# Performance work log

Measured on AMD Instinct MI355X. Metric: run time of the kernel, lower is better.

Reference implementation:

```python
import jax, jax.numpy as jnp
import numpy as np

NUM_HEADS = 12
TOP_K = 2
ROPE_THETA = 10000.0
EPS = 1e-6

def _rmsnorm(x, w):
    return x * jax.lax.rsqrt(jnp.mean(x * x, axis=-1, keepdims=True) + EPS) * w

def _rotate_half(t):
    t1, t2 = jnp.split(t, 2, axis=-1)
    return jnp.concatenate([-t2, t1], axis=-1)

def setup_inputs() -> dict:
    key = jax.random.key(0)
    ks = jax.random.split(key, 8)
    B, S, H, E, F = 2, 2048, 768, 8, 3072
    s = 0.02
    return {
        "x": jax.random.normal(ks[0], (B, S, H), dtype=jnp.float32),
        "attn_norm_w": jnp.ones((H,), dtype=jnp.float32),
        "wqkv": jax.random.normal(ks[1], (H, 3 * H), dtype=jnp.float32) * s,
        "wo": jax.random.normal(ks[2], (H, H), dtype=jnp.float32) * s,
        "ffn_norm_w": jnp.ones((H,), dtype=jnp.float32),
        "router_w": jax.random.normal(ks[3], (H, E), dtype=jnp.float32) * s,
        "w1": jax.random.normal(ks[4], (E, H, F), dtype=jnp.float32) * s,
        "w2": jax.random.normal(ks[5], (E, F, H), dtype=jnp.float32) * s,
    }

def reference(x, attn_norm_w, wqkv, wo, ffn_norm_w, router_w, w1, w2):
    B, S, H = x.shape
    NH, Dh = NUM_HEADS, H // NUM_HEADS
    E = router_w.shape[1]

    # ---- attention sub-block: x = x + attn(rmsnorm(x)) ----
    h = _rmsnorm(x, attn_norm_w)
    qkv = h @ wqkv  # (B,S,3H)
    q, k, v = [t.reshape(B, S, NH, Dh) for t in jnp.split(qkv, 3, axis=-1)]

    # RoPE (llama-style half-split rotation)
    half = Dh // 2
    inv_freq = 1.0 / (ROPE_THETA ** (jnp.arange(half, dtype=jnp.float32) / half))
    ang = jnp.arange(S, dtype=jnp.float32)[:, None] * inv_freq[None, :]  # (S, half)
    cos = jnp.concatenate([jnp.cos(ang)] * 2, axis=-1)[None, :, None, :].astype(x.dtype)
    sin = jnp.concatenate([jnp.sin(ang)] * 2, axis=-1)[None, :, None, :].astype(x.dtype)
    q = q * cos + _rotate_half(q) * sin
    k = k * cos + _rotate_half(k) * sin

    scores = jnp.einsum('bqhd,bkhd->bhqk', q, k) / jnp.sqrt(jnp.asarray(Dh, x.dtype))
    causal = jnp.tril(jnp.ones((S, S), dtype=bool))
    scores = jnp.where(causal[None, None], scores, jnp.asarray(-1e9, x.dtype))
    attn = jax.nn.softmax(scores, axis=-1)
    o = jnp.einsum('bhqk,bkhd->bqhd', attn, v).reshape(B, S, H) @ wo
    x = x + o

    # ---- MoE FFN sub-block: x = x + moe(rmsnorm(x)) ----
    hn = _rmsnorm(x, ffn_norm_w).reshape(-1, H)  # (T,H)
    logits = hn @ router_w  # (T,E)
    probs = jax.nn.softmax(logits, axis=-1)
    top_v, top_i = jax.lax.top_k(probs, TOP_K)  # (T,K)
    top_v = top_v / jnp.sum(top_v, axis=-1, keepdims=True)
    onehot = jax.nn.one_hot(top_i, E, dtype=x.dtype)  # (T,K,E)
    combine = jnp.einsum('tke,tk->te', onehot, top_v)  # (T,E)

    h1 = jnp.einsum('th,ehf->etf', hn, w1)
    h2 = jnp.einsum('etf,efh->eth', jax.nn.silu(h1), w2)
    moe_out = jnp.einsum('eth,te->th', h2, combine).reshape(B, S, H)

    # load-balancing aux loss (switch-style)
    frac = jnp.mean(jnp.sum(onehot, axis=1), axis=0) / TOP_K  # (E,)
    mean_prob = jnp.mean(probs, axis=0)  # (E,)
    aux = jnp.asarray(E, x.dtype) * jnp.sum(frac * mean_prob)

    return (x + moe_out, aux)
```

## Files before the change

kernel.cpp:

```cpp
#include <hip/hip_runtime.h>
#include <cstdint>
#include <cstddef>

typedef __bf16 bf16;
typedef bf16 bf16x8 __attribute__((ext_vector_type(8)));
typedef bf16 bf16x4 __attribute__((ext_vector_type(4)));
typedef float f32x4 __attribute__((ext_vector_type(4)));

static constexpr size_t SKS = (size_t)10240 * 768;

template <int N> struct ICst { static constexpr int v = N; };

__device__ __forceinline__ void async_cp16(const void* g, void* l) {
    __builtin_amdgcn_global_load_lds(
        (const __attribute__((address_space(1))) unsigned int*)(unsigned long long)g,
        (__attribute__((address_space(3))) unsigned int*)(unsigned int)(unsigned long long)l,
        16, 0, 0);
}

#define BARX() __builtin_amdgcn_s_barrier()
#define LGKM0() asm volatile("s_waitcnt lgkmcnt(0)" ::: "memory")
#define VMC8() asm volatile("s_waitcnt vmcnt(8)" ::: "memory")
#define VMC0() asm volatile("s_waitcnt vmcnt(0)" ::: "memory")

__global__ __launch_bounds__(256) void transpose_cast(const float* __restrict__ in,
                                                      bf16* __restrict__ out, int R, int C) {
    __shared__ float tile[32][33];
    int bz = blockIdx.z;
    in  += (size_t)bz * R * C;
    out += (size_t)bz * R * C;
    int c0 = blockIdx.x * 32, r0 = blockIdx.y * 32;
    int lr = threadIdx.x >> 3, lc = (threadIdx.x & 7) * 4;
    float4 v = *(const float4*)&in[(size_t)(r0 + lr) * C + c0 + lc];
    tile[lr][lc] = v.x; tile[lr][lc + 1] = v.y; tile[lr][lc + 2] = v.z; tile[lr][lc + 3] = v.w;
    __syncthreads();
    int sc = threadIdx.x >> 3, sr = (threadIdx.x & 7) * 4;
    bf16x4 o;
    o[0] = (bf16)tile[sr][sc]; o[1] = (bf16)tile[sr + 1][sc];
    o[2] = (bf16)tile[sr + 2][sc]; o[3] = (bf16)tile[sr + 3][sc];
    *(bf16x4*)&out[(size_t)(c0 + sc) * R + r0 + sr] = o;
}

__global__ __launch_bounds__(256) void rmsnorm_cast(const float* __restrict__ x,
                                                    const float* __restrict__ w,
                                                    bf16* __restrict__ out) {
    int row = blockIdx.x, tid = threadIdx.x;
    const float* xr = x + (size_t)row * 768;
    float v0 = xr[tid], v1 = xr[tid + 256], v2 = xr[tid + 512];
    float s = v0 * v0 + v1 * v1 + v2 * v2;
#pragma unroll
    for (int off = 32; off; off >>= 1) s += __shfl_xor(s, off, 64);
    __shared__ float red[4];
    if ((tid & 63) == 0) red[tid >> 6] = s;
    __syncthreads();
    float tot = red[0] + red[1] + red[2] + red[3];
    float rs = rsqrtf(tot * (1.f / 768.f) + 1e-6f);
    bf16* o = out + (size_t)row * 768;
    o[tid]       = (bf16)(v0 * rs * w[tid]);
    o[tid + 256] = (bf16)(v1 * rs * w[tid + 256]);
    o[tid + 512] = (bf16)(v2 * rs * w[tid + 512]);
}

__global__ __launch_bounds__(256) void rope_kernel(const bf16* __restrict__ qkv,
                                                   bf16* __restrict__ qb,
                                                   bf16* __restrict__ kb,
                                                   bf16* __restrict__ vtb) {
    __shared__ float vs[64][65];
    const int tid = threadIdx.x;
    const int s0 = blockIdx.x * 64, bh = blockIdx.y;
    const int b = bh / 12, h = bh - b * 12;
    const float qscale = 0.18033688f;
#pragma unroll
    for (int i = 0; i < 16; ++i) {
        int idx = i * 256 + tid;
        int sl = idx >> 6, d = idx & 63;
        int sg = s0 + sl;
        size_t base = ((size_t)b * 2048 + sg) * 2304;
        float qv = (float)qkv[base + h * 64 + d];
        float kv = (float)qkv[base + 768 + h * 64 + d];
        float vv = (float)qkv[base + 1536 + h * 64 + d];
        float qp = (float)qkv[base + h * 64 + (d ^ 32)];
        float kp = (float)qkv[base + 768 + h * 64 + (d ^ 32)];
        int jj = d & 31;
        float invf = __expf(-(float)jj * (9.210340371976184f / 32.f));
        float ang = (float)sg * invf;
        float cv, sv;
        __sincosf(ang, &sv, &cv);
        float rq = (d < 32) ? -qp : qp;
        float rk = (d < 32) ? -kp : kp;
        qb[((size_t)bh * 2048 + sg) * 64 + d] = (bf16)((qv * cv + rq * sv) * qscale);
        kb[((size_t)bh * 2048 + sg) * 64 + d] = (bf16)(kv * cv + rk * sv);
        vs[sl][d] = vv;
    }
    __syncthreads();
#pragma unroll
    for (int i = 0; i < 16; ++i) {
        int idx = i * 256 + tid;
        int d = idx >> 6, sl = idx & 63;
        vtb[(size_t)bh * 64 * 2048 + (size_t)d * 2048 + s0 + sl] = (bf16)vs[sl][d];
    }
}

__global__ __launch_bounds__(256) void attn_kernel(const bf16* __restrict__ qb,
                                                   const bf16* __restrict__ kb,
                                                   const bf16* __restrict__ vtb,
                                                   bf16* __restrict__ ob) {
    __shared__ __align__(16) bf16 Qs[2][64][32];
    __shared__ __align__(16) bf16 Ks[2][2][64][32];
    __shared__ __align__(16) bf16 Vts[2][2][64][32];
    __shared__ __align__(16) bf16 Ps[4][1024];

    const int tid = threadIdx.x, lane = tid & 63, w = tid >> 6;
    const int quad = lane >> 4, l16 = lane & 15;
    const int linear = (int)blockIdx.y * 32 + (int)blockIdx.x;
    const int xcd = linear & 7, j = linear >> 3;
    const int bh = xcd * 3 + (j >> 5);
    const int qt = 31 - (j & 31);
    const int q0 = qt * 64;
    const int b = bh / 12, h = bh - b * 12;

    const bf16* qhead = qb + (size_t)bh * 2048 * 64;
    const bf16* khead = kb + (size_t)bh * 2048 * 64;
    const bf16* vthead = vtb + (size_t)bh * 64 * 2048;

#pragma unroll
    for (int i = 0; i < 2; ++i) {
        int o = (i * 256 + tid) * 16;
        int kk = o >> 12, row = (o >> 6) & 63, el = (o & 63) >> 1;
        async_cp16(qhead + (size_t)(q0 + row) * 64 + kk * 32 + el,
                   (char*)Qs + (size_t)(i * 256 + w * 64) * 16);
    }
    __syncthreads();
    bf16x8 bq[2];
#pragma unroll
    for (int kk = 0; kk < 2; ++kk)
        bq[kk] = *(const bf16x8*)&Qs[kk][w * 16 + l16][quad * 8];

    f32x4 o_acc[4] = {};
    float m_st = -1e30f, l_st = 0.f;

    for (int j2 = 0; j2 <= qt; j2 += 2) {
        int nt2 = (j2 + 1 <= qt) ? 2 : 1;
        __syncthreads();
#pragma unroll
        for (int t = 0; t < 2; ++t) {
            if (t >= nt2) break;
            int kv0 = (j2 + t) * 64;
#pragma unroll
            for (int i = 0; i < 2; ++i) {
                int o = (i * 256 + tid) * 16;
                int kk = o >> 12, row = (o >> 6) & 63, el = (o & 63) >> 1;
                async_cp16(khead + (size_t)(kv0 + row) * 64 + kk * 32 + el,
                           (char*)&Ks[t] + (size_t)(i * 256 + w * 64) * 16);
                async_cp16(vthead + (size_t)row * 2048 + kv0 + kk * 32 + el,
                           (char*)&Vts[t] + (size_t)(i * 256 + w * 64) * 16);
            }
        }
        __syncthreads();

#pragma unroll
        for (int t = 0; t < 2; ++t) {
            if (t >= nt2) break;

            f32x4 sacc[4] = {};
#pragma unroll
            for (int kk = 0; kk < 2; ++kk) {
                bf16x8 ak[4];
#pragma unroll
                for (int ni = 0; ni < 4; ++ni)
                    ak[ni] = *(const bf16x8*)&Ks[t][kk][ni * 16 + l16][quad * 8];
#pragma unroll
                for (int ni = 0; ni < 4; ++ni)
                    sacc[ni] = __builtin_amdgcn_mfma_f32_16x16x32_bf16(ak[ni], bq[kk], sacc[ni], 0, 0, 0);
            }

            if (j2 + t == qt) {
                int ql = w * 16 + l16;
#pragma unroll
                for (int ni = 0; ni < 4; ++ni)
#pragma unroll
                    for (int r = 0; r < 4; ++r)
                        if (ni * 16 + quad * 4 + r > ql) sacc[ni][r] = -1e30f;
            }

            float mx = sacc[0][0];
#pragma unroll
            for (int ni = 0; ni < 4; ++ni)
#pragma unroll
                for (int r = 0; r < 4; ++r) mx = fmaxf(mx, sacc[ni][r]);
            mx = fmaxf(mx, __shfl_xor(mx, 16, 64));
            mx = fmaxf(mx, __shfl_xor(mx, 32, 64));
            float mnew = fmaxf(m_st, mx);
            float alpha = exp2f(m_st - mnew);
            m_st = mnew;
            float rsum = 0.f;
#pragma unroll
            for (int ni = 0; ni < 4; ++ni)
#pragma unroll
                for (int r = 0; r < 4; ++r) {
                    float pv = exp2f(sacc[ni][r] - mnew);
                    sacc[ni][r] = pv;
                    rsum += pv;
                }
            rsum += __shfl_xor(rsum, 16, 64);
            rsum += __shfl_xor(rsum, 32, 64);
            l_st = l_st * alpha + rsum;

            float af[4];
#pragma unroll
            for (int r = 0; r < 4; ++r) af[r] = __shfl(alpha, quad * 4 + r, 64);
#pragma unroll
            for (int ni = 0; ni < 4; ++ni)
#pragma unroll
                for (int r = 0; r < 4; ++r) o_acc[ni][r] *= af[r];

            bf16* pb = Ps[w];
#pragma unroll
            for (int ni = 0; ni < 4; ++ni)
#pragma unroll
                for (int r = 0; r < 4; ++r) {
                    int kv = ni * 16 + quad * 4 + r;
                    int ch = (kv >> 3) ^ (l16 & 7);
                    pb[l16 * 64 + ch * 8 + (kv & 7)] = (bf16)sacc[ni][r];
                }

#pragma unroll
            for (int kk = 0; kk < 2; ++kk) {
                int ch = (kk * 4 + quad) ^ (l16 & 7);
                bf16x8 ap = *(const bf16x8*)&pb[l16 * 64 + ch * 8];
                bf16x8 bv[4];
#pragma unroll
                for (int ni = 0; ni < 4; ++ni)
                    bv[ni] = *(const bf16x8*)&Vts[t][kk][ni * 16 + l16][quad * 8];
#pragma unroll
                for (int ni = 0; ni < 4; ++ni)
                    o_acc[ni] = __builtin_amdgcn_mfma_f32_16x16x32_bf16(ap, bv[ni], o_acc[ni], 0, 0, 0);
            }
        }
    }

    float lf[4];
#pragma unroll
    for (int r = 0; r < 4; ++r) lf[r] = 1.f / __shfl(l_st, quad * 4 + r, 64);
#pragma unroll
    for (int ni = 0; ni < 4; ++ni)
#pragma unroll
        for (int r = 0; r < 4; ++r) {
            int rowg = q0 + w * 16 + quad * 4 + r;
            size_t tk = (size_t)b * 2048 + rowg;
            ob[tk * 768 + h * 64 + ni * 16 + l16] = (bf16)(o_acc[ni][r] * lf[r]);
        }
}

__global__ __launch_bounds__(256) void rms_router(const float* __restrict__ x1,
                                                  const float* __restrict__ w,
                                                  const float* __restrict__ rw,
                                                  bf16* __restrict__ hn,
                                                  int* __restrict__ topi,
                                                  float* __restrict__ topw,
                                                  float* __restrict__ probsb) {
    __shared__ float hnf[768];
    __shared__ float part[256];
    __shared__ float lg[8];
    __shared__ float probs[8];
    __shared__ float red[4];
    int row = blockIdx.x, tid = threadIdx.x;
    const float* xr = x1 + (size_t)row * 768;
    float v0 = xr[tid], v1 = xr[tid + 256], v2 = xr[tid + 512];
    float s = v0 * v0 + v1 * v1 + v2 * v2;
#pragma unroll
    for (int off = 32; off; off >>= 1) s += __shfl_xor(s, off, 64);
    if ((tid & 63) == 0) red[tid >> 6] = s;
    __syncthreads();
    float tot = red[0] + red[1] + red[2] + red[3];
    float rs = rsqrtf(tot * (1.f / 768.f) + 1e-6f);
    float h0 = v0 * rs * w[tid], h1v = v1 * rs * w[tid + 256], h2v = v2 * rs * w[tid + 512];
    hnf[tid] = h0; hnf[tid + 256] = h1v; hnf[tid + 512] = h2v;
    bf16* o = hn + (size_t)row * 768;
    o[tid] = (bf16)h0; o[tid + 256] = (bf16)h1v; o[tid + 512] = (bf16)h2v;
    __syncthreads();
    int e = tid & 7, seg = tid >> 3;
    float p = 0.f;
#pragma unroll
    for (int j = 0; j < 24; ++j) { int k = seg * 24 + j; p += hnf[k] * rw[k * 8 + e]; }
    part[tid] = p;
    __syncthreads();
    if (tid < 8) { float a = 0.f; for (int sgi = 0; sgi < 32; ++sgi) a += part[sgi * 8 + tid]; lg[tid] = a; }
    __syncthreads();
    if (tid == 0) {
        float mx = lg[0];
        for (int i = 1; i < 8; ++i) mx = fmaxf(mx, lg[i]);
        float ssum = 0.f, ex[8];
        for (int i = 0; i < 8; ++i) { ex[i] = __expf(lg[i] - mx); ssum += ex[i]; }
        float inv = 1.f / ssum;
        for (int i = 0; i < 8; ++i) probs[i] = ex[i] * inv;
        int e0 = 0; float p0 = probs[0];
        for (int i = 1; i < 8; ++i) if (probs[i] > p0) { p0 = probs[i]; e0 = i; }
        int e1 = -1; float p1 = -1.f;
        for (int i = 0; i < 8; ++i) if (i != e0 && probs[i] > p1) { p1 = probs[i]; e1 = i; }
        float wsum = p0 + p1;
        topi[row * 2] = e0; topi[row * 2 + 1] = e1;
        topw[row * 2] = p0 / wsum; topw[row * 2 + 1] = p1 / wsum;
    }
    __syncthreads();
    if (tid < 8) probsb[(size_t)row * 8 + tid] = probs[tid];
}

__global__ __launch_bounds__(256) void router_stats(const float* __restrict__ probsb,
                                                    const int* __restrict__ topi,
                                                    int* ctrl, int4* tiles, float* auxOut) {
    __shared__ float pws[4][8];
    __shared__ int cws[4][8];
    int tid = threadIdx.x;
    float s[8] = {};
    int cnt[8] = {};
    for (int t = tid; t < 4096; t += 256) {
        const float4* p = (const float4*)(probsb + (size_t)t * 8);
        float4 a = p[0], b = p[1];
        s[0] += a.x; s[1] += a.y; s[2] += a.z; s[3] += a.w;
        s[4] += b.x; s[5] += b.y; s[6] += b.z; s[7] += b.w;
        int e0 = topi[2 * t], e1 = topi[2 * t + 1];
#pragma unroll
        for (int e = 0; e < 8; ++e) cnt[e] += (e == e0) + (e == e1);
    }
#pragma unroll
    for (int e = 0; e < 8; ++e)
#pragma unroll
        for (int off = 32; off; off >>= 1) {
            s[e] += __shfl_xor(s[e], off, 64);
            cnt[e] += __shfl_xor(cnt[e], off, 64);
        }
    if ((tid & 63) == 0) {
#pragma unroll
        for (int e = 0; e < 8; ++e) { pws[tid >> 6][e] = s[e]; cws[tid >> 6][e] = cnt[e]; }
    }
    __syncthreads();
    if (tid == 0) {
        int off = 0, nt = 0;
        float aux = 0.f;
        for (int e = 0; e < 8; ++e) {
            int ne = cws[0][e] + cws[1][e] + cws[2][e] + cws[3][e];
            float ps = pws[0][e] + pws[1][e] + pws[2][e] + pws[3][e];
            ctrl[e] = ne;
            ctrl[32 + e] = off;
            int ntl = (ne + 255) >> 8;
            for (int i = 0; i < ntl; ++i) { tiles[nt] = make_int4(e, off + i * 256, off + ne, 0); ++nt; }
            off += ntl << 8;
            aux += ((float)ne * (1.f / 8192.f)) * (ps * (1.f / 4096.f));
        }
        ctrl[24] = nt;
        auxOut[0] = 8.f * aux;
    }
}

__global__ __launch_bounds__(256) void place_tokens(const int* __restrict__ topi,
                                                    int* ctrl, int* __restrict__ perm,
                                                    int* __restrict__ tokslot) {
    __shared__ int lcnt[8], lbase[8];
    int tid = threadIdx.x;
    int t = blockIdx.x * 256 + tid;
    if (tid < 8) lcnt[tid] = 0;
    __syncthreads();
    int e0 = topi[2 * t], e1 = topi[2 * t + 1];
    int p0 = atomicAdd(&lcnt[e0], 1);
    int p1 = atomicAdd(&lcnt[e1], 1);
    __syncthreads();
    if (tid < 8) lbase[tid] = atomicAdd(&ctrl[16 + tid], lcnt[tid]);
    __syncthreads();
    int g0 = ctrl[32 + e0] + lbase[e0] + p0;
    int g1 = ctrl[32 + e1] + lbase[e1] + p1;
    perm[g0] = t; perm[g1] = t;
    tokslot[2 * t] = g0; tokslot[2 * t + 1] = g1;
}

__global__ __launch_bounds__(192) void moe_combine(const float* __restrict__ h2p,
                                                   const int* __restrict__ tokslot,
                                                   const float* __restrict__ topw,
                                                   float* __restrict__ out) {
    int t = blockIdx.x, tid = threadIdx.x;
    int s0 = tokslot[2 * t], s1 = tokslot[2 * t + 1];
    float w0 = topw[2 * t], w1 = topw[2 * t + 1];
    int c = tid * 4;
    float4 a0 = *(const float4*)(h2p + (size_t)s0 * 768 + c);
    float4 a1 = *(const float4*)(h2p + SKS + (size_t)s0 * 768 + c);
    float4 b0 = *(const float4*)(h2p + (size_t)s1 * 768 + c);
    float4 b1 = *(const float4*)(h2p + SKS + (size_t)s1 * 768 + c);
    float4* o = (float4*)(out + (size_t)t * 768 + c);
    float4 ov = *o;
    ov.x += w0 * (a0.x + a1.x) + w1 * (b0.x + b1.x);
    ov.y += w0 * (a0.y + a1.y) + w1 * (b0.y + b1.y);
    ov.z += w0 * (a0.z + a1.z) + w1 * (b0.z + b1.z);
    ov.w += w0 * (a0.w + a1.w) + w1 * (b0.w + b1.w);
    *o = ov;
}

template <int MODE, int KTOT, int SK>
__global__ __launch_bounds__(512, 2) void gemm8p(const bf16* __restrict__ A,
                                                 const bf16* __restrict__ Bt,
                                                 int N,
                                                 bf16* __restrict__ outB,
                                                 float* __restrict__ outF,
                                                 const int4* __restrict__ tiles,
                                                 const int* __restrict__ ctrl,
                                                 const int* __restrict__ perm) {
    constexpr int KB = KTOT / SK;
    constexpr int nT = KB >> 6;
    __shared__ __align__(16) bf16 As[2][2][128 * 64];
    __shared__ __align__(16) bf16 Bs[2][2][128 * 64];
    __shared__ int sPerm[256];

    const int tid = threadIdx.x, lane = tid & 63, wid = tid >> 6;
    const int wr = wid >> 2, wc = wid & 3;
    const int quad = lane >> 4, l16 = lane & 15;

    const int NB = N >> 8;
    const int nwg = (int)gridDim.x, q8 = nwg >> 3;
    const int L = (int)blockIdx.x;
    const int lin = (L & 7) * q8 + (L >> 3);
    int mt, nb, sk = 0;
    if (SK == 2) { int d = NB * 2; mt = lin / d; int r = lin - mt * d; nb = r >> 1; sk = r & 1; }
    else         { mt = lin / NB; nb = lin - mt * NB; }
    const int n0 = nb << 8;
    const int k0 = sk * KB;

    int m0 = 0, row0 = 0;
    if (MODE == 0) {
        m0 = mt << 8;
    } else {
        if (mt >= ctrl[24]) return;
        int4 td = tiles[mt];
        row0 = td.y;
        Bt += (size_t)td.x * (size_t)N * KTOT;
        if (MODE == 2) {
            if (tid < 256) {
                int g = row0 + tid;
                sPerm[tid] = perm[(g < td.z) ? g : row0];
            }
            __syncthreads();
        }
    }

    const int r0t = tid >> 3, s0t = tid & 7;
    const int cOff = ((s0t ^ (r0t & 7)) << 3);
    unsigned aOff[2][2], bOff[2][2];
#pragma unroll
    for (int h = 0; h < 2; ++h)
#pragma unroll
        for (int i = 0; i < 2; ++i) {
            int rrow = h * 128 + i * 64 + r0t;
            bOff[h][i] = (unsigned)((((n0 + rrow) * KTOT) + k0 + cOff) * 2);
            int ar = (MODE == 0) ? (m0 + rrow) : (MODE == 2 ? sPerm[rrow] : row0 + rrow);
            aOff[h][i] = (unsigned)(((ar * KTOT) + k0 + cOff) * 2);
        }
    const char* Ab = (const char*)A;
    const char* Bb = (const char*)Bt;

    auto stA = [&](int buf, int ktB) {
#pragma unroll
        for (int h = 0; h < 2; ++h)
#pragma unroll
            for (int i = 0; i < 2; ++i)
                async_cp16(Ab + aOff[h][i] + ktB,
                           (char*)As[buf][h] + (size_t)((i * 512 + wid * 64) * 16));
    };
    auto stB = [&](int buf, int ktB) {
#pragma unroll
        for (int h = 0; h < 2; ++h)
#pragma unroll
            for (int i = 0; i < 2; ++i)
                async_cp16(Bb + bOff[h][i] + ktB,
                           (char*)Bs[buf][h] + (size_t)((i * 512 + wid * 64) * 16));
    };

    const bf16* aP[2][2];
    const bf16* bP[2][2];
#pragma unroll
    for (int bb = 0; bb < 2; ++bb)
#pragma unroll
        for (int kk = 0; kk < 2; ++kk) {
            int swz = ((kk * 4 + quad) ^ (l16 & 7)) * 8;
            aP[bb][kk] = (const bf16*)As[bb][wr] + l16 * 64 + swz;
            bP[bb][kk] = (const bf16*)Bs[bb][wc >> 1] + ((wc & 1) * 64 + l16) * 64 + swz;
        }

    f32x4 acc[8][4] = {};
    bf16x8 aLo[4][2], aHi[4][2], bLo[2][2], bHi[2][2];

    stA(0, 0); stB(0, 0); stA(1, 128); stB(1, 128);
    VMC8();
    BARX();

    auto dotile = [&](auto BC, int t) {
        constexpr int b = decltype(BC)::v;
        const bool st = (t + 2 < nT);
        const int ktB = (t + 2) << 7;

#pragma unroll
        for (int mi = 0; mi < 4; ++mi) {
            aLo[mi][0] = *(const bf16x8*)(aP[b][0] + mi * 1024);
            aLo[mi][1] = *(const bf16x8*)(aP[b][1] + mi * 1024);
        }
#pragma unroll
        for (int ni = 0; ni < 2; ++ni) {
            bLo[ni][0] = *(const bf16x8*)(bP[b][0] + ni * 1024);
            bLo[ni][1] = *(const bf16x8*)(bP[b][1] + ni * 1024);
        }
        BARX(); LGKM0();
        __builtin_amdgcn_s_setprio(1);
#pragma unroll
        for (int mi = 0; mi < 4; ++mi)
#pragma unroll
            for (int ni = 0; ni < 2; ++ni) {
                acc[mi][ni] = __builtin_amdgcn_mfma_f32_16x16x32_bf16(aLo[mi][0], bLo[ni][0], acc[mi][ni], 0, 0, 0);
                acc[mi][ni] = __builtin_amdgcn_mfma_f32_16x16x32_bf16(aLo[mi][1], bLo[ni][1], acc[mi][ni], 0, 0, 0);
            }
        __builtin_amdgcn_s_setprio(0);
        BARX();

#pragma unroll
        for (int ni = 0; ni < 2; ++ni) {
            bHi[ni][0] = *(const bf16x8*)(bP[b][0] + (ni + 2) * 1024);
            bHi[ni][1] = *(const bf16x8*)(bP[b][1] + (ni + 2) * 1024);
        }
        BARX(); LGKM0();
        __builtin_amdgcn_s_setprio(1);
#pragma unroll
        for (int mi = 0; mi < 4; ++mi)
#pragma unroll
            for (int ni = 0; ni < 2; ++ni) {
                acc[mi][ni + 2] = __builtin_amdgcn_mfma_f32_16x16x32_bf16(aLo[mi][0], bHi[ni][0], acc[mi][ni + 2], 0, 0, 0);
                acc[mi][ni + 2] = __builtin_amdgcn_mfma_f32_16x16x32_bf16(aLo[mi][1], bHi[ni][1], acc[mi][ni + 2], 0, 0, 0);
            }
        __builtin_amdgcn_s_setprio(0);
        BARX();

#pragma unroll
        for (int mi = 0; mi < 4; ++mi) {
            aHi[mi][0] = *(const bf16x8*)(aP[b][0] + (mi + 4) * 1024);
            aHi[mi][1] = *(const bf16x8*)(aP[b][1] + (mi + 4) * 1024);
        }
        if (st) stB(b, ktB);
        BARX(); LGKM0();
        __builtin_amdgcn_s_setprio(1);
#pragma unroll
        for (int mi = 0; mi < 4; ++mi)
#pragma unroll
            for (int ni = 0; ni < 2; ++ni) {
                acc[mi + 4][ni + 2] = __builtin_amdgcn_mfma_f32_16x16x32_bf16(aHi[mi][0], bHi[ni][0], acc[mi + 4][ni + 2], 0, 0, 0);
                acc[mi + 4][ni + 2] = __builtin_amdgcn_mfma_f32_16x16x32_bf16(aHi[mi][1], bHi[ni][1], acc[mi + 4][ni + 2], 0, 0, 0);
            }
        __builtin_amdgcn_s_setprio(0);
        BARX();

        if (st) stA(b, ktB);
        BARX();
        __builtin_amdgcn_s_setprio(1);
#pragma unroll
        for (int mi = 0; mi < 4; ++mi)
#pragma unroll
            for (int ni = 0; ni < 2; ++ni) {
                acc[mi + 4][ni] = __builtin_amdgcn_mfma_f32_16x16x32_bf16(aHi[mi][0], bLo[ni][0], acc[mi + 4][ni], 0, 0, 0);
                acc[mi + 4][ni] = __builtin_amdgcn_mfma_f32_16x16x32_bf16(aHi[mi][1], bLo[ni][1], acc[mi + 4][ni], 0, 0, 0);
            }
        __builtin_amdgcn_s_setprio(0);
        if (st) { VMC8(); } else if (t + 2 == nT) { VMC0(); }
        BARX();
    };

    for (int t = 0; t < nT; t += 2) {
        dotile(ICst<0>{}, t);
        dotile(ICst<1>{}, t + 1);
    }

#pragma unroll
    for (int mi = 0; mi < 8; ++mi)
#pragma unroll
        for (int ni = 0; ni < 4; ++ni)
#pragma unroll
            for (int r = 0; r < 4; ++r) {
                int lrow = wr * 128 + mi * 16 + quad * 4 + r;
                int col  = n0 + wc * 64 + ni * 16 + l16;
                float v = acc[mi][ni][r];
                if (MODE == 0) {
                    outB[(size_t)(m0 + lrow) * N + col] = (bf16)v;
                } else if (MODE == 2) {
                    float sv = v / (1.f + __expf(-v));
                    outB[(size_t)(row0 + lrow) * N + col] = (bf16)sv;
                } else {
                    outF[(size_t)sk * SKS + (size_t)(row0 + lrow) * N + col] = v;
                }
            }
}

template <int MODE, int NBX, int MTX>
__global__ __launch_bounds__(256) void gemm_nt(const bf16* __restrict__ A,
                                               const bf16* __restrict__ Bt,
                                               int N, int K,
                                               const float* __restrict__ xres,
                                               float* __restrict__ outF,
                                               bf16* __restrict__ outB) {
    __shared__ __align__(16) bf16 As[2][128 * 32];
    __shared__ __align__(16) bf16 Bs[2][128 * 32];

    const int tid = threadIdx.x, lane = tid & 63, w = tid >> 6;
    const int wr = w >> 1, wc = w & 1, quad = lane >> 4, l16 = lane & 15;

    const int L = blockIdx.x;
    const int xcd = L & 7, j = L >> 3;
    const int mt = xcd * MTX + j / NBX;
    const int n0 = (j % NBX) * 128;
    const int m0 = mt * 128;

    auto stage = [&](int buf, int kt) {
#pragma unroll
        for (int i = 0; i < 2; ++i) {
            int c = i * 256 + tid;
            int r = c >> 2, koff = (c & 3) * 8;
            async_cp16(A + (size_t)(m0 + r) * K + kt + koff,
                       (char*)As[buf] + (size_t)(i * 256 + w * 64) * 16);
            async_cp16(Bt + (size_t)(n0 + r) * K + kt + koff,
                       (char*)Bs[buf] + (size_t)(i * 256 + w * 64) * 16);
        }
    };

    f32x4 acc[4][4] = {};
    const int nIt = K >> 5;
    stage(0, 0);

    for (int it = 0; it < nIt; ++it) {
        const int cur = it & 1;
        __syncthreads();
        if (it + 1 < nIt) stage(cur ^ 1, (it + 1) << 5);

        bf16x8 af[4], bfr[4];
#pragma unroll
        for (int mi = 0; mi < 4; ++mi)
            af[mi] = *(const bf16x8*)(As[cur] + (wr * 64 + mi * 16 + l16) * 32 + quad * 8);
#pragma unroll
        for (int ni = 0; ni < 4; ++ni)
            bfr[ni] = *(const bf16x8*)(Bs[cur] + (wc * 64 + ni * 16 + l16) * 32 + quad * 8);
#pragma unroll
        for (int mi = 0; mi < 4; ++mi)
#pragma unroll
            for (int ni = 0; ni < 4; ++ni)
                acc[mi][ni] = __builtin_amdgcn_mfma_f32_16x16x32_bf16(af[mi], bfr[ni], acc[mi][ni], 0, 0, 0);
    }

#pragma unroll
    for (int mi = 0; mi < 4; ++mi)
#pragma unroll
        for (int ni = 0; ni < 4; ++ni)
#pragma unroll
            for (int r = 0; r < 4; ++r) {
                int lrow = wr * 64 + mi * 16 + quad * 4 + r;
                int col = n0 + wc * 64 + ni * 16 + l16;
                float v = acc[mi][ni][r];
                if (MODE == 1) {
                    size_t idx = (size_t)(m0 + lrow) * N + col;
                    outF[idx] = v + xres[idx];
                } else {
                    outB[(size_t)(m0 + lrow) * N + col] = (bf16)v;
                }
            }
}

__global__ void zero_ctrl(int* ctrl) { if (threadIdx.x < 64) ctrl[threadIdx.x] = 0; }

extern "C" void kernel_launch(void* const* d_in, const int* in_sizes, int n_in,
                              void* d_out, int out_size, void* d_ws, size_t ws_size,
                              hipStream_t stream) {
    const float* x    = (const float*)d_in[0];
    const float* anw  = (const float*)d_in[1];
    const float* wqkv = (const float*)d_in[2];
    const float* wo   = (const float*)d_in[3];
    const float* fnw  = (const float*)d_in[4];
    const float* rw   = (const float*)d_in[5];
    const float* w1   = (const float*)d_in[6];
    const float* w2   = (const float*)d_in[7];
    float* out = (float*)d_out;

    char* ws = (char*)d_ws;
    size_t off = 0;
    auto alloc = [&](size_t bytes) -> char* {
        char* p = ws + off;
        off = (off + bytes + 255) & ~(size_t)255;
        return p;
    };
    bf16* wqkvT = (bf16*)alloc(2304ull * 768 * 2);
    bf16* woT   = (bf16*)alloc(768ull * 768 * 2);
    bf16* w2T   = (bf16*)alloc(8ull * 768 * 3072 * 2);
    bf16* w1T   = (bf16*)alloc(8ull * 3072 * 768 * 2);
    bf16* hbuf  = (bf16*)alloc(4096ull * 768 * 2);
    bf16* qkvb  = (bf16*)alloc(4096ull * 2304 * 2);
    bf16* qb    = (bf16*)alloc(24ull * 2048 * 64 * 2);
    bf16* kb    = (bf16*)alloc(24ull * 2048 * 64 * 2);
    bf16* vtb   = (bf16*)alloc(24ull * 64 * 2048 * 2);
    bf16* obuf  = (bf16*)alloc(4096ull * 768 * 2);
    bf16* hn    = (bf16*)alloc(4096ull * 768 * 2);
    int*  topi  = (int*)alloc(4096ull * 2 * 4);
    float* topw = (float*)alloc(4096ull * 2 * 4);
    float* probsb = (float*)alloc(4096ull * 8 * 4);
    int*  ctrl  = (int*)alloc(64 * 4);
    int4* tiles = (int4*)alloc(80 * 16);
    int*  perm  = (int*)alloc(10240 * 4);
    int*  tokslot = (int*)alloc(4096ull * 2 * 4);
    bf16* h1    = (bf16*)alloc(10240ull * 3072 * 2);
    float* h2p  = (float*)w1T;
    (void)ws_size; (void)in_sizes; (void)n_in;

    zero_ctrl<<<1, 64, 0, stream>>>(ctrl);
    transpose_cast<<<dim3(72, 24, 1), 256, 0, stream>>>(wqkv, wqkvT, 768, 2304);
    transpose_cast<<<dim3(24, 24, 1), 256, 0, stream>>>(wo, woT, 768, 768);
    transpose_cast<<<dim3(96, 24, 8), 256, 0, stream>>>(w1, w1T, 768, 3072);
    transpose_cast<<<dim3(24, 96, 8), 256, 0, stream>>>(w2, w2T, 3072, 768);
    rmsnorm_cast<<<4096, 256, 0, stream>>>(x, anw, hbuf);
    gemm8p<0, 768, 1><<<144, 512, 0, stream>>>(hbuf, wqkvT, 2304, qkvb, nullptr,
                                               nullptr, nullptr, nullptr);
    rope_kernel<<<dim3(32, 24), 256, 0, stream>>>(qkvb, qb, kb, vtb);
    attn_kernel<<<dim3(32, 24), 256, 0, stream>>>(qb, kb, vtb, obuf);
    gemm_nt<1, 6, 4><<<192, 256, 0, stream>>>(obuf, woT, 768, 768, x, out, nullptr);
    rms_router<<<4096, 256, 0, stream>>>(out, fnw, rw, hn, topi, topw, probsb);
    router_stats<<<1, 256, 0, stream>>>(probsb, topi, ctrl, tiles, out + (out_size - 1));
    place_tokens<<<16, 256, 0, stream>>>(topi, ctrl, perm, tokslot);
    gemm8p<2, 768, 1><<<480, 512, 0, stream>>>(hn, w1T, 3072, h1, nullptr,
                                               tiles, ctrl, perm);
    gemm8p<3, 3072, 2><<<240, 512, 0, stream>>>(h1, w2T, 768, nullptr, h2p,
                                                tiles, ctrl, perm);
    moe_combine<<<4096, 192, 0, stream>>>(h2p, tokslot, topw, out);
}
```

Measured before the change: 500.2 us.

## Load GEMM A operand directly into registers, stage only B through LDS

The 256x256 GEMM kernel stops staging the A tile through shared memory. Each wave now reads its A rows straight from global memory into registers, one k-step ahead, while B keeps its double-buffered async LDS copies. The per-tile schedule shrinks to two MFMA phases with fewer barriers. Workgroup swizzling is dropped for the MoE modes. This removes LDS traffic and barriers for A, but adds register pressure (16 bf16x8 A fragments live per wave) and exposes global-load latency, since A is fetched with uncoalesced 16-byte per-lane reads right before use.

```diff
diff --git a/kernel.cpp b/kernel.cpp
--- a/kernel.cpp
+++ b/kernel.cpp
@@ -19,8 +19,8 @@
 }
 
 #define BARX() __builtin_amdgcn_s_barrier()
-#define LGKM0() asm volatile("s_waitcnt lgkmcnt(0)" ::: "memory")
-#define VMC8() asm volatile("s_waitcnt vmcnt(8)" ::: "memory")
+#define SBAR0() __builtin_amdgcn_sched_barrier(0)
+#define VMC4() asm volatile("s_waitcnt vmcnt(4)" ::: "memory")
 #define VMC0() asm volatile("s_waitcnt vmcnt(0)" ::: "memory")
 
 __global__ __launch_bounds__(256) void transpose_cast(const float* __restrict__ in,
@@ -395,7 +395,7 @@
 }
 
 template <int MODE, int KTOT, int SK>
-__global__ __launch_bounds__(512, 2) void gemm8p(const bf16* __restrict__ A,
+__global__ __launch_bounds__(512, 2) void gemm2p(const bf16* __restrict__ A,
                                                  const bf16* __restrict__ Bt,
                                                  int N,
                                                  bf16* __restrict__ outB,
@@ -405,7 +405,6 @@
                                                  const int* __restrict__ perm) {
     constexpr int KB = KTOT / SK;
     constexpr int nT = KB >> 6;
-    __shared__ __align__(16) bf16 As[2][2][128 * 64];
     __shared__ __align__(16) bf16 Bs[2][2][128 * 64];
     __shared__ int sPerm[256];
 
@@ -414,9 +413,14 @@
     const int quad = lane >> 4, l16 = lane & 15;
 
     const int NB = N >> 8;
-    const int nwg = (int)gridDim.x, q8 = nwg >> 3;
     const int L = (int)blockIdx.x;
-    const int lin = (L & 7) * q8 + (L >> 3);
+    int lin;
+    if (MODE == 0) {
+        const int q8 = (int)gridDim.x >> 3;
+        lin = (L & 7) * q8 + (L >> 3);
+    } else {
+        lin = L;
+    }
     int mt, nb, sk = 0;
     if (SK == 2) { int d = NB * 2; mt = lin / d; int r = lin - mt * d; nb = r >> 1; sk = r & 1; }
     else         { mt = lin / NB; nb = lin - mt * NB; }
@@ -442,27 +446,16 @@
 
     const int r0t = tid >> 3, s0t = tid & 7;
     const int cOff = ((s0t ^ (r0t & 7)) << 3);
-    unsigned aOff[2][2], bOff[2][2];
+    unsigned bOff[2][2];
 #pragma unroll
     for (int h = 0; h < 2; ++h)
 #pragma unroll
         for (int i = 0; i < 2; ++i) {
             int rrow = h * 128 + i * 64 + r0t;
             bOff[h][i] = (unsigned)((((n0 + rrow) * KTOT) + k0 + cOff) * 2);
-            int ar = (MODE == 0) ? (m0 + rrow) : (MODE == 2 ? sPerm[rrow] : row0 + rrow);
-            aOff[h][i] = (unsigned)(((ar * KTOT) + k0 + cOff) * 2);
-        }
-    const char* Ab = (const char*)A;
+        }
     const char* Bb = (const char*)Bt;
 
-    auto stA = [&](int buf, int ktB) {
-#pragma unroll
-        for (int h = 0; h < 2; ++h)
-#pragma unroll
-            for (int i = 0; i < 2; ++i)
-                async_cp16(Ab + aOff[h][i] + ktB,
-                           (char*)As[buf][h] + (size_t)((i * 512 + wid * 64) * 16));
-    };
     auto stB = [&](int buf, int ktB) {
 #pragma unroll
         for (int h = 0; h < 2; ++h)
@@ -472,99 +465,88 @@
                            (char*)Bs[buf][h] + (size_t)((i * 512 + wid * 64) * 16));
     };
 
-    const bf16* aP[2][2];
     const bf16* bP[2][2];
 #pragma unroll
     for (int bb = 0; bb < 2; ++bb)
 #pragma unroll
         for (int kk = 0; kk < 2; ++kk) {
             int swz = ((kk * 4 + quad) ^ (l16 & 7)) * 8;
-            aP[bb][kk] = (const bf16*)As[bb][wr] + l16 * 64 + swz;
             bP[bb][kk] = (const bf16*)Bs[bb][wc >> 1] + ((wc & 1) * 64 + l16) * 64 + swz;
         }
 
+    const char* aPtr[8];
+#pragma unroll
+    for (int mi = 0; mi < 8; ++mi) {
+        int lrow = wr * 128 + mi * 16 + l16;
+        int rowIdx = (MODE == 0) ? (m0 + lrow) : (MODE == 2 ? sPerm[lrow] : row0 + lrow);
+        aPtr[mi] = (const char*)A + (size_t)((unsigned)rowIdx * (unsigned)KTOT + (unsigned)(k0 + quad * 8)) * 2;
+    }
+
     f32x4 acc[8][4] = {};
-    bf16x8 aLo[4][2], aHi[4][2], bLo[2][2], bHi[2][2];
-
-    stA(0, 0); stB(0, 0); stA(1, 128); stB(1, 128);
-    VMC8();
-    BARX();
+    bf16x8 aCur[8][2];
+
+    auto loadA = [&](int ktB) {
+#pragma unroll
+        for (int mi = 0; mi < 8; ++mi)
+#pragma unroll
+            for (int kk = 0; kk < 2; ++kk)
+                aCur[mi][kk] = *(const bf16x8*)(aPtr[mi] + ktB + kk * 64);
+    };
+
+    stB(0, 0);
+    SBAR0();
+    loadA(0);
+    SBAR0();
+    stB(1, 128);
+    SBAR0();
 
     auto dotile = [&](auto BC, int t) {
         constexpr int b = decltype(BC)::v;
-        const bool st = (t + 2 < nT);
-        const int ktB = (t + 2) << 7;
-
-#pragma unroll
-        for (int mi = 0; mi < 4; ++mi) {
-            aLo[mi][0] = *(const bf16x8*)(aP[b][0] + mi * 1024);
-            aLo[mi][1] = *(const bf16x8*)(aP[b][1] + mi * 1024);
-        }
+        const bool lastT = (t == nT - 1);
+
+        if (lastT) { VMC0(); } else { VMC4(); }
+        BARX();
+        SBAR0();
+
+        bf16x8 bLo[2][2];
 #pragma unroll
         for (int ni = 0; ni < 2; ++ni) {
             bLo[ni][0] = *(const bf16x8*)(bP[b][0] + ni * 1024);
             bLo[ni][1] = *(const bf16x8*)(bP[b][1] + ni * 1024);
         }
-        BARX(); LGKM0();
         __builtin_amdgcn_s_setprio(1);
 #pragma unroll
-        for (int mi = 0; mi < 4; ++mi)
+        for (int mi = 0; mi < 8; ++mi)
 #pragma unroll
             for (int ni = 0; ni < 2; ++ni) {
-                acc[mi][ni] = __builtin_amdgcn_mfma_f32_16x16x32_bf16(aLo[mi][0], bLo[ni][0], acc[mi][ni], 0, 0, 0);
-                acc[mi][ni] = __builtin_amdgcn_mfma_f32_16x16x32_bf16(aLo[mi][1], bLo[ni][1], acc[mi][ni], 0, 0, 0);
+                acc[mi][ni] = __builtin_amdgcn_mfma_f32_16x16x32_bf16(aCur[mi][0], bLo[ni][0], acc[mi][ni], 0, 0, 0);
+                acc[mi][ni] = __builtin_amdgcn_mfma_f32_16x16x32_bf16(aCur[mi][1], bLo[ni][1], acc[mi][ni], 0, 0, 0);
             }
         __builtin_amdgcn_s_setprio(0);
-        BARX();
-
+
+        bf16x8 bHi[2][2];
 #pragma unroll
         for (int ni = 0; ni < 2; ++ni) {
             bHi[ni][0] = *(const bf16x8*)(bP[b][0] + (ni + 2) * 1024);
             bHi[ni][1] = *(const bf16x8*)(bP[b][1] + (ni + 2) * 1024);
         }
-        BARX(); LGKM0();
         __builtin_amdgcn_s_setprio(1);
 #pragma unroll
-        for (int mi = 0; mi < 4; ++mi)
+        for (int mi = 0; mi < 8; ++mi)
 #pragma unroll
             for (int ni = 0; ni < 2; ++ni) {
-                acc[mi][ni + 2] = __builtin_amdgcn_mfma_f32_16x16x32_bf16(aLo[mi][0], bHi[ni][0], acc[mi][ni + 2], 0, 0, 0);
-                acc[mi][ni + 2] = __builtin_amdgcn_mfma_f32_16x16x32_bf16(aLo[mi][1], bHi[ni][1], acc[mi][ni + 2], 0, 0, 0);
+                acc[mi][ni + 2] = __builtin_amdgcn_mfma_f32_16x16x32_bf16(aCur[mi][0], bHi[ni][0], acc[mi][ni + 2], 0, 0, 0);
+                acc[mi][ni + 2] = __builtin_amdgcn_mfma_f32_16x16x32_bf16(aCur[mi][1], bHi[ni][1], acc[mi][ni + 2], 0, 0, 0);
             }
         __builtin_amdgcn_s_setprio(0);
+
+        SBAR0();
         BARX();
-
-#pragma unroll
-        for (int mi = 0; mi < 4; ++mi) {
-            aHi[mi][0] = *(const bf16x8*)(aP[b][0] + (mi + 4) * 1024);
-            aHi[mi][1] = *(const bf16x8*)(aP[b][1] + (mi + 4) * 1024);
-        }
-        if (st) stB(b, ktB);
-        BARX(); LGKM0();
-        __builtin_amdgcn_s_setprio(1);
-#pragma unroll
-        for (int mi = 0; mi < 4; ++mi)
-#pragma unroll
-            for (int ni = 0; ni < 2; ++ni) {
-                acc[mi + 4][ni + 2] = __builtin_amdgcn_mfma_f32_16x16x32_bf16(aHi[mi][0], bHi[ni][0], acc[mi + 4][ni + 2], 0, 0, 0);
-                acc[mi + 4][ni + 2] = __builtin_amdgcn_mfma_f32_16x16x32_bf16(aHi[mi][1], bHi[ni][1], acc[mi + 4][ni + 2], 0, 0, 0);
-            }
-        __builtin_amdgcn_s_setprio(0);
-        BARX();
-
-        if (st) stA(b, ktB);
-        BARX();
-        __builtin_amdgcn_s_setprio(1);
-#pragma unroll
-        for (int mi = 0; mi < 4; ++mi)
-#pragma unroll
-            for (int ni = 0; ni < 2; ++ni) {
-                acc[mi + 4][ni] = __builtin_amdgcn_mfma_f32_16x16x32_bf16(aHi[mi][0], bLo[ni][0], acc[mi + 4][ni], 0, 0, 0);
-                acc[mi + 4][ni] = __builtin_amdgcn_mfma_f32_16x16x32_bf16(aHi[mi][1], bLo[ni][1], acc[mi + 4][ni], 0, 0, 0);
-            }
-        __builtin_amdgcn_s_setprio(0);
-        if (st) { VMC8(); } else if (t + 2 == nT) { VMC0(); }
-        BARX();
+        if (!lastT) {
+            loadA((t + 1) << 7);
+            SBAR0();
+            if (t + 2 < nT) { stB(b, (t + 2) << 7); SBAR0(); }
+        }
     };
 
     for (int t = 0; t < nT; t += 2) {
@@ -714,7 +696,7 @@
     transpose_cast<<<dim3(96, 24, 8), 256, 0, stream>>>(w1, w1T, 768, 3072);
     transpose_cast<<<dim3(24, 96, 8), 256, 0, stream>>>(w2, w2T, 3072, 768);
     rmsnorm_cast<<<4096, 256, 0, stream>>>(x, anw, hbuf);
-    gemm8p<0, 768, 1><<<144, 512, 0, stream>>>(hbuf, wqkvT, 2304, qkvb, nullptr,
+    gemm2p<0, 768, 1><<<144, 512, 0, stream>>>(hbuf, wqkvT, 2304, qkvb, nullptr,
                                                nullptr, nullptr, nullptr);
     rope_kernel<<<dim3(32, 24), 256, 0, stream>>>(qkvb, qb, kb, vtb);
     attn_kernel<<<dim3(32, 24), 256, 0, stream>>>(qb, kb, vtb, obuf);
@@ -722,9 +704,9 @@
     rms_router<<<4096, 256, 0, stream>>>(out, fnw, rw, hn, topi, topw, probsb);
     router_stats<<<1, 256, 0, stream>>>(probsb, topi, ctrl, tiles, out + (out_size - 1));
     place_tokens<<<16, 256, 0, stream>>>(topi, ctrl, perm, tokslot);
-    gemm8p<2, 768, 1><<<480, 512, 0, stream>>>(hn, w1T, 3072, h1, nullptr,
+    gemm2p<2, 768, 1><<<480, 512, 0, stream>>>(hn, w1T, 3072, h1, nullptr,
                                                tiles, ctrl, perm);
-    gemm8p<3, 3072, 2><<<240, 512, 0, stream>>>(h1, w2T, 768, nullptr, h2p,
+    gemm2p<3, 3072, 2><<<240, 512, 0, stream>>>(h1, w2T, 768, nullptr, h2p,
                                                 tiles, ctrl, perm);
     moe_combine<<<4096, 192, 0, stream>>>(h2p, tokslot, topw, out);
 }
```

After: 699.2 us. +39.8%, slower.

## Fuse prep kernels and overlap expert weight transposes with attention

Applied to the files above, without the earlier changes.

Merges the zero-ctrl, wqkv/wo transpose-casts and the first rmsnorm into a single launch. The large w1/w2 expert-weight transpose-cast blocks are appended to the attention grid, so the bandwidth-bound conversion can fill CUs left idle by the causal, imbalanced attention blocks. This cuts several launches and hides the weight conversion behind attention. The risk is that the many transpose blocks compete with attention for bandwidth and CU slots, and the shared-memory union may lower attention occupancy.

```diff
diff --git a/kernel.cpp b/kernel.cpp
--- a/kernel.cpp
+++ b/kernel.cpp
@@ -23,42 +23,54 @@
 #define VMC8() asm volatile("s_waitcnt vmcnt(8)" ::: "memory")
 #define VMC0() asm volatile("s_waitcnt vmcnt(0)" ::: "memory")
 
-__global__ __launch_bounds__(256) void transpose_cast(const float* __restrict__ in,
-                                                      bf16* __restrict__ out, int R, int C) {
-    __shared__ float tile[32][33];
-    int bz = blockIdx.z;
-    in  += (size_t)bz * R * C;
-    out += (size_t)bz * R * C;
-    int c0 = blockIdx.x * 32, r0 = blockIdx.y * 32;
-    int lr = threadIdx.x >> 3, lc = (threadIdx.x & 7) * 4;
+__device__ __forceinline__ void tc_body(const float* __restrict__ in, bf16* __restrict__ out,
+                                        int R, int C, int r0, int c0, float* shf) {
+    float (*tile)[33] = (float(*)[33])shf;
+    int tid = threadIdx.x;
+    int lr = tid >> 3, lc = (tid & 7) * 4;
     float4 v = *(const float4*)&in[(size_t)(r0 + lr) * C + c0 + lc];
     tile[lr][lc] = v.x; tile[lr][lc + 1] = v.y; tile[lr][lc + 2] = v.z; tile[lr][lc + 3] = v.w;
     __syncthreads();
-    int sc = threadIdx.x >> 3, sr = (threadIdx.x & 7) * 4;
+    int sc = tid >> 3, sr = (tid & 7) * 4;
     bf16x4 o;
     o[0] = (bf16)tile[sr][sc]; o[1] = (bf16)tile[sr + 1][sc];
     o[2] = (bf16)tile[sr + 2][sc]; o[3] = (bf16)tile[sr + 3][sc];
     *(bf16x4*)&out[(size_t)(c0 + sc) * R + r0 + sr] = o;
 }
 
-__global__ __launch_bounds__(256) void rmsnorm_cast(const float* __restrict__ x,
-                                                    const float* __restrict__ w,
-                                                    bf16* __restrict__ out) {
-    int row = blockIdx.x, tid = threadIdx.x;
-    const float* xr = x + (size_t)row * 768;
-    float v0 = xr[tid], v1 = xr[tid + 256], v2 = xr[tid + 512];
-    float s = v0 * v0 + v1 * v1 + v2 * v2;
-#pragma unroll
-    for (int off = 32; off; off >>= 1) s += __shfl_xor(s, off, 64);
-    __shared__ float red[4];
-    if ((tid & 63) == 0) red[tid >> 6] = s;
-    __syncthreads();
-    float tot = red[0] + red[1] + red[2] + red[3];
-    float rs = rsqrtf(tot * (1.f / 768.f) + 1e-6f);
-    bf16* o = out + (size_t)row * 768;
-    o[tid]       = (bf16)(v0 * rs * w[tid]);
-    o[tid + 256] = (bf16)(v1 * rs * w[tid + 256]);
-    o[tid + 512] = (bf16)(v2 * rs * w[tid + 512]);
+__global__ __launch_bounds__(256) void prep1(const float* __restrict__ x,
+                                             const float* __restrict__ anw,
+                                             bf16* __restrict__ hbuf,
+                                             const float* __restrict__ wqkv,
+                                             bf16* __restrict__ wqkvT,
+                                             const float* __restrict__ wo,
+                                             bf16* __restrict__ woT,
+                                             int* __restrict__ ctrl) {
+    __shared__ __align__(16) float shf[32 * 33];
+    const int bid = (int)blockIdx.x, tid = threadIdx.x;
+    if (bid < 4096) {
+        const float* xr = x + (size_t)bid * 768;
+        float v0 = xr[tid], v1 = xr[tid + 256], v2 = xr[tid + 512];
+        float s = v0 * v0 + v1 * v1 + v2 * v2;
+#pragma unroll
+        for (int off = 32; off; off >>= 1) s += __shfl_xor(s, off, 64);
+        if ((tid & 63) == 0) shf[tid >> 6] = s;
+        __syncthreads();
+        float tot = shf[0] + shf[1] + shf[2] + shf[3];
+        float rs = rsqrtf(tot * (1.f / 768.f) + 1e-6f);
+        bf16* o = hbuf + (size_t)bid * 768;
+        o[tid]       = (bf16)(v0 * rs * anw[tid]);
+        o[tid + 256] = (bf16)(v1 * rs * anw[tid + 256]);
+        o[tid + 512] = (bf16)(v2 * rs * anw[tid + 512]);
+    } else if (bid < 5824) {
+        int i = bid - 4096;
+        tc_body(wqkv, wqkvT, 768, 2304, (i / 72) * 32, (i % 72) * 32, shf);
+    } else if (bid < 6400) {
+        int i = bid - 5824;
+        tc_body(wo, woT, 768, 768, (i / 24) * 32, (i % 24) * 32, shf);
+    } else {
+        if (tid < 64) ctrl[tid] = 0;
+    }
 }
 
 __global__ __launch_bounds__(256) void rope_kernel(const bf16* __restrict__ qkv,
@@ -101,18 +113,43 @@
     }
 }
 
-__global__ __launch_bounds__(256) void attn_kernel(const bf16* __restrict__ qb,
-                                                   const bf16* __restrict__ kb,
-                                                   const bf16* __restrict__ vtb,
-                                                   bf16* __restrict__ ob) {
-    __shared__ __align__(16) bf16 Qs[2][64][32];
-    __shared__ __align__(16) bf16 Ks[2][2][64][32];
-    __shared__ __align__(16) bf16 Vts[2][2][64][32];
-    __shared__ __align__(16) bf16 Ps[4][1024];
+struct AttnSh {
+    bf16 Qs[2][64][32];
+    bf16 Ks[2][2][64][32];
+    bf16 Vts[2][2][64][32];
+    bf16 Ps[4][1024];
+};
+union ShU { AttnSh a; float tile[32 * 33]; };
+
+__global__ __launch_bounds__(256) void attn_tw(const bf16* __restrict__ qb,
+                                               const bf16* __restrict__ kb,
+                                               const bf16* __restrict__ vtb,
+                                               bf16* __restrict__ ob,
+                                               const float* __restrict__ w1,
+                                               bf16* __restrict__ w1T,
+                                               const float* __restrict__ w2,
+                                               bf16* __restrict__ w2T) {
+    __shared__ __align__(16) ShU sh;
+    const int bid = (int)blockIdx.x;
+
+    if (bid >= 768) {
+        int i = bid - 768;
+        if (i < 18432) {
+            int bz = i / 2304, r = i - bz * 2304;
+            tc_body(w1 + (size_t)bz * 768 * 3072, w1T + (size_t)bz * 768 * 3072,
+                    768, 3072, ((r / 96) % 24) * 32, (r % 96) * 32, sh.tile);
+        } else {
+            i -= 18432;
+            int bz = i / 2304, r = i - bz * 2304;
+            tc_body(w2 + (size_t)bz * 3072 * 768, w2T + (size_t)bz * 3072 * 768,
+                    3072, 768, ((r / 24) % 96) * 32, (r % 24) * 32, sh.tile);
+        }
+        return;
+    }
 
     const int tid = threadIdx.x, lane = tid & 63, w = tid >> 6;
     const int quad = lane >> 4, l16 = lane & 15;
-    const int linear = (int)blockIdx.y * 32 + (int)blockIdx.x;
+    const int linear = bid;
     const int xcd = linear & 7, j = linear >> 3;
     const int bh = xcd * 3 + (j >> 5);
     const int qt = 31 - (j & 31);
@@ -128,13 +165,13 @@
         int o = (i * 256 + tid) * 16;
         int kk = o >> 12, row = (o >> 6) & 63, el = (o & 63) >> 1;
         async_cp16(qhead + (size_t)(q0 + row) * 64 + kk * 32 + el,
-                   (char*)Qs + (size_t)(i * 256 + w * 64) * 16);
+                   (char*)sh.a.Qs + (size_t)(i * 256 + w * 64) * 16);
     }
     __syncthreads();
     bf16x8 bq[2];
 #pragma unroll
     for (int kk = 0; kk < 2; ++kk)
-        bq[kk] = *(const bf16x8*)&Qs[kk][w * 16 + l16][quad * 8];
+        bq[kk] = *(const bf16x8*)&sh.a.Qs[kk][w * 16 + l16][quad * 8];
 
     f32x4 o_acc[4] = {};
     float m_st = -1e30f, l_st = 0.f;
@@ -151,9 +188,9 @@
                 int o = (i * 256 + tid) * 16;
                 int kk = o >> 12, row = (o >> 6) & 63, el = (o & 63) >> 1;
                 async_cp16(khead + (size_t)(kv0 + row) * 64 + kk * 32 + el,
-                           (char*)&Ks[t] + (size_t)(i * 256 + w * 64) * 16);
+                           (char*)&sh.a.Ks[t] + (size_t)(i * 256 + w * 64) * 16);
                 async_cp16(vthead + (size_t)row * 2048 + kv0 + kk * 32 + el,
-                           (char*)&Vts[t] + (size_t)(i * 256 + w * 64) * 16);
+                           (char*)&sh.a.Vts[t] + (size_t)(i * 256 + w * 64) * 16);
             }
         }
         __syncthreads();
@@ -168,7 +205,7 @@
                 bf16x8 ak[4];
 #pragma unroll
                 for (int ni = 0; ni < 4; ++ni)
-                    ak[ni] = *(const bf16x8*)&Ks[t][kk][ni * 16 + l16][quad * 8];
+                    ak[ni] = *(const bf16x8*)&sh.a.Ks[t][kk][ni * 16 + l16][quad * 8];
 #pragma unroll
                 for (int ni = 0; ni < 4; ++ni)
                     sacc[ni] = __builtin_amdgcn_mfma_f32_16x16x32_bf16(ak[ni], bq[kk], sacc[ni], 0, 0, 0);
@@ -214,7 +251,7 @@
 #pragma unroll
                 for (int r = 0; r < 4; ++r) o_acc[ni][r] *= af[r];
 
-            bf16* pb = Ps[w];
+            bf16* pb = sh.a.Ps[w];
 #pragma unroll
             for (int ni = 0; ni < 4; ++ni)
 #pragma unroll
@@ -231,7 +268,7 @@
                 bf16x8 bv[4];
 #pragma unroll
                 for (int ni = 0; ni < 4; ++ni)
-                    bv[ni] = *(const bf16x8*)&Vts[t][kk][ni * 16 + l16][quad * 8];
+                    bv[ni] = *(const bf16x8*)&sh.a.Vts[t][kk][ni * 16 + l16][quad * 8];
 #pragma unroll
                 for (int ni = 0; ni < 4; ++ni)
                     o_acc[ni] = __builtin_amdgcn_mfma_f32_16x16x32_bf16(ap, bv[ni], o_acc[ni], 0, 0, 0);
@@ -663,8 +700,6 @@
                 }
             }
 }
-
-__global__ void zero_ctrl(int* ctrl) { if (threadIdx.x < 64) ctrl[threadIdx.x] = 0; }
 
 extern "C" void kernel_launch(void* const* d_in, const int* in_sizes, int n_in,
                               void* d_out, int out_size, void* d_ws, size_t ws_size,
@@ -708,16 +743,11 @@
     float* h2p  = (float*)w1T;
     (void)ws_size; (void)in_sizes; (void)n_in;
 
-    zero_ctrl<<<1, 64, 0, stream>>>(ctrl);
-    transpose_cast<<<dim3(72, 24, 1), 256, 0, stream>>>(wqkv, wqkvT, 768, 2304);
-    transpose_cast<<<dim3(24, 24, 1), 256, 0, stream>>>(wo, woT, 768, 768);
-    transpose_cast<<<dim3(96, 24, 8), 256, 0, stream>>>(w1, w1T, 768, 3072);
-    transpose_cast<<<dim3(24, 96, 8), 256, 0, stream>>>(w2, w2T, 3072, 768);
-    rmsnorm_cast<<<4096, 256, 0, stream>>>(x, anw, hbuf);
+    prep1<<<6401, 256, 0, stream>>>(x, anw, hbuf, wqkv, wqkvT, wo, woT, ctrl);
     gemm8p<0, 768, 1><<<144, 512, 0, stream>>>(hbuf, wqkvT, 2304, qkvb, nullptr,
                                                nullptr, nullptr, nullptr);
     rope_kernel<<<dim3(32, 24), 256, 0, stream>>>(qkvb, qb, kb, vtb);
-    attn_kernel<<<dim3(32, 24), 256, 0, stream>>>(qb, kb, vtb, obuf);
+    attn_tw<<<768 + 36864, 256, 0, stream>>>(qb, kb, vtb, obuf, w1, w1T, w2, w2T);
     gemm_nt<1, 6, 4><<<192, 256, 0, stream>>>(obuf, woT, 768, 768, x, out, nullptr);
     rms_router<<<4096, 256, 0, stream>>>(out, fnw, rw, hn, topi, topw, probsb);
     router_stats<<<1, 256, 0, stream>>>(probsb, topi, ctrl, tiles, out + (out_size - 1));
```

Result: faster. 449.1 us (-10.2%).
